# Performance work log

Measured on AMD Instinct MI355X. Metric: run time of the kernel, lower is better.

The kernel has to match this reference:

```python
import jax, jax.numpy as jnp
import numpy as np

N_NODES = 100000
N_EDGES = 1600000
IN_F = 128
OUT_F = 64
K = 2


def _propagate(x, src, dst, num_nodes):
    """GCN propagation with self-loops already appended to (src, dst).
    out[j] = sum_{(i->j)} deg(i)^-1/2 * deg(j)^-1/2 * x[i]
    where deg is the in-degree counting self-loops (PyG gcn_norm)."""
    deg = jnp.zeros((num_nodes,), dtype=x.dtype).at[dst].add(1.0)
    dinv = jnp.where(deg > 0, jax.lax.rsqrt(deg), 0.0)
    norm = dinv[src] * dinv[dst]                      # [E+N]
    msg = x[src] * norm[:, None]                      # gather + scale
    return jnp.zeros_like(x).at[dst].add(msg)         # scatter-add


def setup_inputs() -> dict:
    key = jax.random.key(0)
    k1, k2, k3, k4 = jax.random.split(key, 4)
    x = jax.random.normal(k1, (N_NODES, IN_F), dtype=jnp.float32)
    edge_index = jax.random.randint(k2, (2, N_EDGES), 0, N_NODES, dtype=jnp.int64)
    # Linear weights, torch convention: y = x @ W.T, W is [out, in]
    W1 = jax.random.normal(k3, (IN_F, IN_F), dtype=jnp.float32) / np.sqrt(IN_F)
    W2 = jax.random.normal(k4, (OUT_F, IN_F), dtype=jnp.float32) / np.sqrt(IN_F)
    return {"x": x, "edge_index": edge_index, "W1": W1, "W2": W2}


def reference(x, edge_index, W1, W2):
    num_nodes = x.shape[0]
    # add self loops once (same augmented edge set used by P1 and P2)
    loop = jnp.arange(num_nodes, dtype=edge_index.dtype)
    src = jnp.concatenate([edge_index[0], loop])
    dst = jnp.concatenate([edge_index[1], loop])
    for _ in range(K):
        x = x @ W1.T
        x = _propagate(x, src, dst, num_nodes)
    x = x @ W2.T
    x = _propagate(x, src, dst, num_nodes)
    # original computes log_softmax into `out` but returns pre-softmax x
    return x
```

## Files before the change

### kernel.cpp

```cpp
#include <hip/hip_runtime.h>

#define NN 100000
#define NE 1600000
#define ENT (NE + NN)
#define NB 196
#define BINCAP 10240


__global__ __launch_bounds__(256) void wprod1_kernel(const float* __restrict__ W1,
                                                     const float* __restrict__ W2,
                                                     float* __restrict__ T,
                                                     const unsigned* __restrict__ edges,
                                                     int* __restrict__ flag,
                                                     int* __restrict__ binCnt) {
    if (blockIdx.x == 0) {
        int t = threadIdx.x;
        if (t < NB) binCnt[t] = 0;
        if (t == 0) {
            int is64 = 1;
            for (int i = 1; i < 64; i += 2)
                if (edges[i] != 0u) { is64 = 0; break; }
            *flag = is64;
        }
    }
    int idx = blockIdx.x * blockDim.x + threadIdx.x;
    if (idx >= 128 * 64) return;
    int k = idx >> 6, j = idx & 63;
    float s = 0.f;
    #pragma unroll 8
    for (int q = 0; q < 128; ++q)
        s += W1[q * 128 + k] * W2[j * 128 + q];
    T[k * 64 + j] = s;
}


__global__ __launch_bounds__(256) void part_kernel(const void* __restrict__ edges,
                                                   const int* __restrict__ flag,
                                                   int* __restrict__ binned,
                                                   int* __restrict__ binCnt,
                                                   const float* __restrict__ W1,
                                                   const float* __restrict__ T,
                                                   float* __restrict__ WcT) {
    __shared__ int hist[NB], base[NB], rank[NB];
    int t = threadIdx.x;
    for (int i = t; i < NB; i += 256) hist[i] = 0;
    __syncthreads();
    int i0 = blockIdx.x * 4096;
    bool is64 = (*flag != 0);
    int s[16], d[16];
    #pragma unroll
    for (int q = 0; q < 16; ++q) {
        int i = i0 + q * 256 + t;
        if (i < NE) {
            if (is64) {
                s[q] = (int)__builtin_nontemporal_load(&((const long long*)edges)[i]);
                d[q] = (int)__builtin_nontemporal_load(&((const long long*)edges)[NE + i]);
            } else {
                s[q] = __builtin_nontemporal_load(&((const int*)edges)[i]);
                d[q] = __builtin_nontemporal_load(&((const int*)edges)[NE + i]);
            }
            atomicAdd(&hist[d[q] >> 9], 1);
        } else d[q] = -1;
    }
    __syncthreads();
    for (int i = t; i < NB; i += 256) {
        base[i] = atomicAdd(&binCnt[i], hist[i]);
        rank[i] = 0;
    }
    __syncthreads();
    #pragma unroll
    for (int q = 0; q < 16; ++q) {
        if (d[q] >= 0) {
            int b = d[q] >> 9;
            int r = base[b] + atomicAdd(&rank[b], 1);
            if (r < BINCAP)
                binned[(size_t)b * BINCAP + r] = ((d[q] & 511) << 17) | s[q];
        }
    }
    if (blockIdx.x < 32) {
        int idx = blockIdx.x * 256 + t;
        int i = idx >> 6, j = idx & 63;
        float sum = 0.f;
        #pragma unroll 8
        for (int k = 0; k < 128; ++k)
            sum += W1[k * 128 + i] * T[k * 64 + j];
        WcT[j * 128 + i] = sum;
    }
}


__global__ __launch_bounds__(1024) void build2_kernel(const int* __restrict__ binCnt,
                                                      const int* __restrict__ binned,
                                                      float* __restrict__ dinv,
                                                      int* __restrict__ rowoff,
                                                      int* __restrict__ edge) {
    extern __shared__ char smem[];
    int* stage = (int*)smem;
    int* hist  = (int*)(smem + (size_t)BINCAP * 4);
    int* sc    = hist + 512;
    int* cur   = sc + 512;
    int* bsc   = cur + 512;
    int b = blockIdx.x, t = threadIdx.x;
    int nb0 = b << 9;
    int nNodes = min(512, NN - nb0);

    if (t < 256) {
        int nodes = (t < NB) ? min(512, NN - (t << 9)) : 0;
        bsc[t] = (t < NB) ? binCnt[t] + nodes : 0;
    }
    if (t < 512) hist[t] = 0;
    __syncthreads();
    for (int off = 1; off < 256; off <<= 1) {
        int a = (t < 256 && t >= off) ? bsc[t - off] : 0;
        __syncthreads();
        if (t < 256) bsc[t] += a;
        __syncthreads();
    }
    int cntRaw = binCnt[b];
    int cnt = min(cntRaw, BINCAP);
    int off0 = bsc[b] - (cntRaw + nNodes);

    const int* e = binned + (size_t)b * BINCAP;
    for (int i = t; i < cnt; i += 1024) atomicAdd(&hist[e[i] >> 17], 1);
    __syncthreads();
    int v = 0;
    if (t < 512) { v = (t < nNodes) ? hist[t] + 1 : 0; sc[t] = v; }
    __syncthreads();
    for (int off = 1; off < 512; off <<= 1) {
        int a = (t < 512 && t >= off) ? sc[t - off] : 0;
        __syncthreads();
        if (t < 512) sc[t] += a;
        __syncthreads();
    }
    if (t < nNodes) {
        dinv[nb0 + t] = rsqrtf((float)(hist[t] + 1));
        int lo = sc[t] - v;
        rowoff[nb0 + t] = off0 + lo;
        stage[lo] = nb0 + t;
        cur[t] = lo + 1;
    }
    if (b == NB - 1 && t == 0) rowoff[NN] = ENT;
    __syncthreads();
    for (int i = t; i < cnt; i += 1024) {
        int pk = e[i];
        int slot = atomicAdd(&cur[pk >> 17], 1);
        if (slot < BINCAP) stage[slot] = pk & 0x1FFFF;
    }
    __syncthreads();
    int total = min(cntRaw + nNodes, BINCAP);
    int* dst = edge + off0;
    for (int i = t; i < total; i += 1024) dst[i] = stage[i];
}


template<int SPOW>
__global__ __launch_bounds__(256) void spmm64f_kernel(const int* __restrict__ rowoff,
                                                      const int* __restrict__ col,
                                                      const float* __restrict__ dinv,
                                                      const float* __restrict__ H,
                                                      float* __restrict__ O) {
    int w = (int)((blockIdx.x * (unsigned)blockDim.x + threadIdx.x) >> 6);
    if (w >= NN) return;
    int lane = threadIdx.x & 63;
    int s = __builtin_amdgcn_readfirstlane(rowoff[w]);
    int e = __builtin_amdgcn_readfirstlane(rowoff[w + 1]);
    float acc = 0.f;
    const float* base = H + lane;

    int p = s;
    for (; p + 16 <= e; p += 16) {
        int c[16];
        #pragma unroll
        for (int q = 0; q < 16; ++q) c[q] = __builtin_nontemporal_load(&col[p + q]);
        #pragma unroll
        for (int q = 0; q < 16; ++q) acc += base[(size_t)c[q] * 64];
    }
    if (p + 8 <= e) {
        int c[8];
        #pragma unroll
        for (int q = 0; q < 8; ++q) c[q] = __builtin_nontemporal_load(&col[p + q]);
        #pragma unroll
        for (int q = 0; q < 8; ++q) acc += base[(size_t)c[q] * 64];
        p += 8;
    }
    if (p + 4 <= e) {
        int c[4];
        #pragma unroll
        for (int q = 0; q < 4; ++q) c[q] = __builtin_nontemporal_load(&col[p + q]);
        #pragma unroll
        for (int q = 0; q < 4; ++q) acc += base[(size_t)c[q] * 64];
        p += 4;
    }
    for (; p < e; ++p) acc += base[(size_t)__builtin_nontemporal_load(&col[p]) * 64];

    float di = dinv[w];
    float scale = (SPOW == 2) ? di * di : di;
    __builtin_nontemporal_store(acc * scale, &O[(size_t)w * 64 + lane]);
}


__global__ __launch_bounds__(256) void gemm_xwt64_kernel(const float* __restrict__ X,
                                                         const float* __restrict__ W,
                                                         const float* __restrict__ dinv,
                                                         float* __restrict__ Y, int M) {
    constexpr int N = 64, K = 128, BM = 64, BK = 32;
    constexpr int TM = 4, TN = N / 16;
    __shared__ float Xs[BK][BM + 4];
    __shared__ float Ws[BK][N + 4];
    int t  = threadIdx.x;
    int m0 = blockIdx.x * BM;
    int r0 = (t >> 4) * TM;
    int c0 = (t & 15) * TN;
    float acc[TM][TN] = {};
    for (int k0 = 0; k0 < K; k0 += BK) {
        #pragma unroll
        for (int i = 0; i < 2; ++i) {
            int f  = t + i * 256;
            int m  = f >> 3;
            int kq = (f & 7) << 2;
            int gm = m0 + m; if (gm >= M) gm = M - 1;
            float4 v;
            v.x = __builtin_nontemporal_load(&X[(size_t)gm * K + k0 + kq + 0]);
            v.y = __builtin_nontemporal_load(&X[(size_t)gm * K + k0 + kq + 1]);
            v.z = __builtin_nontemporal_load(&X[(size_t)gm * K + k0 + kq + 2]);
            v.w = __builtin_nontemporal_load(&X[(size_t)gm * K + k0 + kq + 3]);
            Xs[kq + 0][m] = v.x; Xs[kq + 1][m] = v.y;
            Xs[kq + 2][m] = v.z; Xs[kq + 3][m] = v.w;
        }
        #pragma unroll
        for (int i = 0; i < N / 32; ++i) {
            int f  = t + i * 256;
            int n  = f >> 3;
            int kq = (f & 7) << 2;
            float4 v = *(const float4*)&W[(size_t)n * K + k0 + kq];
            Ws[kq + 0][n] = v.x; Ws[kq + 1][n] = v.y;
            Ws[kq + 2][n] = v.z; Ws[kq + 3][n] = v.w;
        }
        __syncthreads();
        #pragma unroll
        for (int k = 0; k < BK; ++k) {
            float4 xv = *(const float4*)&Xs[k][r0];
            float xf[TM] = {xv.x, xv.y, xv.z, xv.w};
            float wf[TN];
            #pragma unroll
            for (int j = 0; j < TN; j += 4) {
                float4 wv = *(const float4*)&Ws[k][c0 + j];
                wf[j] = wv.x; wf[j + 1] = wv.y; wf[j + 2] = wv.z; wf[j + 3] = wv.w;
            }
            #pragma unroll
            for (int i = 0; i < TM; ++i)
                #pragma unroll
                for (int j = 0; j < TN; ++j)
                    acc[i][j] += xf[i] * wf[j];
        }
        __syncthreads();
    }
    #pragma unroll
    for (int i = 0; i < TM; ++i) {
        int gm = m0 + r0 + i;
        if (gm < M) {
            float di = dinv[gm];
            #pragma unroll
            for (int j = 0; j < TN; ++j)
                __builtin_nontemporal_store(di * acc[i][j],
                                            &Y[(size_t)gm * N + c0 + j]);
        }
    }
}


extern "C" void kernel_launch(void* const* d_in, const int* in_sizes, int n_in,
                              void* d_out, int out_size, void* d_ws, size_t ws_size,
                              hipStream_t stream) {
    const float* x     = (const float*)d_in[0];
    const void*  edges = d_in[1];
    const float* W1    = (const float*)d_in[2];
    const float* W2    = (const float*)d_in[3];
    float* out = (float*)d_out;

    char* ws = (char*)d_ws;
    size_t off = 0;
    auto take = [&](size_t bytes) -> char* {
        char* p = ws + off;
        off = (off + bytes + 255) & ~(size_t)255;
        return p;
    };
    int*   flag   = (int*)take(4);
    int*   binCnt = (int*)take((size_t)NB * 4);
    float* dinv   = (float*)take((size_t)NN * 4);
    int*   rowoff = (int*)take((size_t)(NN + 1) * 4);
    float* Tbuf   = (float*)take((size_t)128 * 64 * 4);
    float* WcT    = (float*)take((size_t)64 * 128 * 4);
    int*   binned = (int*)take((size_t)NB * BINCAP * 4);
    int*   edgeA  = (int*)take((size_t)ENT * 4);
    float* g      = (float*)take((size_t)NN * 64 * 4);
    float* y      = (float*)take((size_t)NN * 64 * 4);
    if (off > ws_size) return;

    wprod1_kernel<<<32, 256, 0, stream>>>(W1, W2, Tbuf, (const unsigned*)edges, flag, binCnt);
    part_kernel<<<(NE + 4095) / 4096, 256, 0, stream>>>(edges, flag, binned, binCnt,
                                                        W1, Tbuf, WcT);
    size_t b2lds = (size_t)BINCAP * 4 + (512 * 3 + 256) * 4;
    build2_kernel<<<NB, 1024, b2lds, stream>>>(binCnt, binned, dinv, rowoff, edgeA);

    const int GB = (NN + 63) / 64;
    const int PB = (NN * 64 + 255) / 256;

    gemm_xwt64_kernel<<<GB, 256, 0, stream>>>(x, WcT, dinv, g, NN);
    spmm64f_kernel<2><<<PB, 256, 0, stream>>>(rowoff, edgeA, dinv, g, y);
    spmm64f_kernel<2><<<PB, 256, 0, stream>>>(rowoff, edgeA, dinv, y, g);
    spmm64f_kernel<1><<<PB, 256, 0, stream>>>(rowoff, edgeA, dinv, g, out);
}
```

Before: 254.0 us.

## Coalesce weight-product loops, vectorize GEMM loads/stores, enlarge SpMM blocks

The small weight-product kernels now map consecutive threads to consecutive columns of W1 and use four partial accumulators, with the intermediate stored transposed so its reads broadcast within a row. The GEMM loads X and stores Y with 128-bit nontemporal vector operations instead of scalar ones. The three SpMM launches switch from 256 to 1024 threads per block, which means fewer blocks with 16 waves each. The weight kernels are tiny, so the main intended effects come from the wider memory operations and the changed SpMM block shape, and the larger blocks may affect occupancy or scheduling granularity.

```diff
diff --git a/kernel.cpp b/kernel.cpp
--- a/kernel.cpp
+++ b/kernel.cpp
@@ -6,10 +6,12 @@
 #define NB 196
 #define BINCAP 10240
 
+typedef float f4v __attribute__((ext_vector_type(4)));
+
 
 __global__ __launch_bounds__(256) void wprod1_kernel(const float* __restrict__ W1,
                                                      const float* __restrict__ W2,
-                                                     float* __restrict__ T,
+                                                     float* __restrict__ T2,
                                                      const unsigned* __restrict__ edges,
                                                      int* __restrict__ flag,
                                                      int* __restrict__ binCnt) {
@@ -24,13 +26,17 @@
         }
     }
     int idx = blockIdx.x * blockDim.x + threadIdx.x;
-    if (idx >= 128 * 64) return;
-    int k = idx >> 6, j = idx & 63;
-    float s = 0.f;
-    #pragma unroll 8
-    for (int q = 0; q < 128; ++q)
-        s += W1[q * 128 + k] * W2[j * 128 + q];
-    T[k * 64 + j] = s;
+    int k = idx & 127;
+    int j = idx >> 7;
+    float s0 = 0.f, s1 = 0.f, s2 = 0.f, s3 = 0.f;
+    #pragma unroll 4
+    for (int q = 0; q < 128; q += 4) {
+        s0 += W1[(q + 0) * 128 + k] * W2[j * 128 + q + 0];
+        s1 += W1[(q + 1) * 128 + k] * W2[j * 128 + q + 1];
+        s2 += W1[(q + 2) * 128 + k] * W2[j * 128 + q + 2];
+        s3 += W1[(q + 3) * 128 + k] * W2[j * 128 + q + 3];
+    }
+    T2[j * 128 + k] = (s0 + s1) + (s2 + s3);
 }
 
 
@@ -39,7 +45,7 @@
                                                    int* __restrict__ binned,
                                                    int* __restrict__ binCnt,
                                                    const float* __restrict__ W1,
-                                                   const float* __restrict__ T,
+                                                   const float* __restrict__ T2,
                                                    float* __restrict__ WcT) {
     __shared__ int hist[NB], base[NB], rank[NB];
     int t = threadIdx.x;
@@ -79,12 +85,17 @@
     }
     if (blockIdx.x < 32) {
         int idx = blockIdx.x * 256 + t;
-        int i = idx >> 6, j = idx & 63;
-        float sum = 0.f;
-        #pragma unroll 8
-        for (int k = 0; k < 128; ++k)
-            sum += W1[k * 128 + i] * T[k * 64 + j];
-        WcT[j * 128 + i] = sum;
+        int i = idx & 127;
+        int j = idx >> 7;
+        float s0 = 0.f, s1 = 0.f, s2 = 0.f, s3 = 0.f;
+        #pragma unroll 4
+        for (int k = 0; k < 128; k += 4) {
+            s0 += W1[(k + 0) * 128 + i] * T2[j * 128 + k + 0];
+            s1 += W1[(k + 1) * 128 + i] * T2[j * 128 + k + 1];
+            s2 += W1[(k + 2) * 128 + i] * T2[j * 128 + k + 2];
+            s3 += W1[(k + 3) * 128 + i] * T2[j * 128 + k + 3];
+        }
+        WcT[j * 128 + i] = (s0 + s1) + (s2 + s3);
     }
 }
 
@@ -154,12 +165,12 @@
 
 
 template<int SPOW>
-__global__ __launch_bounds__(256) void spmm64f_kernel(const int* __restrict__ rowoff,
-                                                      const int* __restrict__ col,
-                                                      const float* __restrict__ dinv,
-                                                      const float* __restrict__ H,
-                                                      float* __restrict__ O) {
-    int w = (int)((blockIdx.x * (unsigned)blockDim.x + threadIdx.x) >> 6);
+__global__ __launch_bounds__(1024) void spmm64f_kernel(const int* __restrict__ rowoff,
+                                                       const int* __restrict__ col,
+                                                       const float* __restrict__ dinv,
+                                                       const float* __restrict__ H,
+                                                       float* __restrict__ O) {
+    int w = (int)((blockIdx.x * 1024u + threadIdx.x) >> 6);
     if (w >= NN) return;
     int lane = threadIdx.x & 63;
     int s = __builtin_amdgcn_readfirstlane(rowoff[w]);
@@ -219,11 +230,8 @@
             int m  = f >> 3;
             int kq = (f & 7) << 2;
             int gm = m0 + m; if (gm >= M) gm = M - 1;
-            float4 v;
-            v.x = __builtin_nontemporal_load(&X[(size_t)gm * K + k0 + kq + 0]);
-            v.y = __builtin_nontemporal_load(&X[(size_t)gm * K + k0 + kq + 1]);
-            v.z = __builtin_nontemporal_load(&X[(size_t)gm * K + k0 + kq + 2]);
-            v.w = __builtin_nontemporal_load(&X[(size_t)gm * K + k0 + kq + 3]);
+            f4v v = __builtin_nontemporal_load(
+                (const f4v*)&X[(size_t)gm * K + k0 + kq]);
             Xs[kq + 0][m] = v.x; Xs[kq + 1][m] = v.y;
             Xs[kq + 2][m] = v.z; Xs[kq + 3][m] = v.w;
         }
@@ -261,9 +269,11 @@
         if (gm < M) {
             float di = dinv[gm];
             #pragma unroll
-            for (int j = 0; j < TN; ++j)
-                __builtin_nontemporal_store(di * acc[i][j],
-                                            &Y[(size_t)gm * N + c0 + j]);
+            for (int j = 0; j < TN; j += 4) {
+                f4v v = {di * acc[i][j], di * acc[i][j + 1],
+                         di * acc[i][j + 2], di * acc[i][j + 3]};
+                __builtin_nontemporal_store(v, (f4v*)&Y[(size_t)gm * N + c0 + j]);
+            }
         }
     }
 }
@@ -289,7 +299,7 @@
     int*   binCnt = (int*)take((size_t)NB * 4);
     float* dinv   = (float*)take((size_t)NN * 4);
     int*   rowoff = (int*)take((size_t)(NN + 1) * 4);
-    float* Tbuf   = (float*)take((size_t)128 * 64 * 4);
+    float* T2     = (float*)take((size_t)64 * 128 * 4);
     float* WcT    = (float*)take((size_t)64 * 128 * 4);
     int*   binned = (int*)take((size_t)NB * BINCAP * 4);
     int*   edgeA  = (int*)take((size_t)ENT * 4);
@@ -297,17 +307,17 @@
     float* y      = (float*)take((size_t)NN * 64 * 4);
     if (off > ws_size) return;
 
-    wprod1_kernel<<<32, 256, 0, stream>>>(W1, W2, Tbuf, (const unsigned*)edges, flag, binCnt);
+    wprod1_kernel<<<32, 256, 0, stream>>>(W1, W2, T2, (const unsigned*)edges, flag, binCnt);
     part_kernel<<<(NE + 4095) / 4096, 256, 0, stream>>>(edges, flag, binned, binCnt,
-                                                        W1, Tbuf, WcT);
+                                                        W1, T2, WcT);
     size_t b2lds = (size_t)BINCAP * 4 + (512 * 3 + 256) * 4;
     build2_kernel<<<NB, 1024, b2lds, stream>>>(binCnt, binned, dinv, rowoff, edgeA);
 
     const int GB = (NN + 63) / 64;
-    const int PB = (NN * 64 + 255) / 256;
+    const int PB = (NN * 64 + 1023) / 1024;
 
     gemm_xwt64_kernel<<<GB, 256, 0, stream>>>(x, WcT, dinv, g, NN);
-    spmm64f_kernel<2><<<PB, 256, 0, stream>>>(rowoff, edgeA, dinv, g, y);
-    spmm64f_kernel<2><<<PB, 256, 0, stream>>>(rowoff, edgeA, dinv, y, g);
-    spmm64f_kernel<1><<<PB, 256, 0, stream>>>(rowoff, edgeA, dinv, g, out);
-}
+    spmm64f_kernel<2><<<PB, 1024, 0, stream>>>(rowoff, edgeA, dinv, g, y);
+    spmm64f_kernel<2><<<PB, 1024, 0, stream>>>(rowoff, edgeA, dinv, y, g);
+    spmm64f_kernel<1><<<PB, 1024, 0, stream>>>(rowoff, edgeA, dinv, g, out);
+}
```

Measured after the change: 258.3 us. No clear change (+1.7%).
